# Performance work log

Measured on AMD Instinct MI355X. Metric: run time of the kernel, lower is better.

Reference implementation:

```python
import jax, jax.numpy as jnp
import numpy as np

N = 100_000   # nodes
E = 1_600_000 # edges
K = 3         # Chebyshev order


def _cheb_norm(row, col, w, n):
    # PyG ChebConv norm with normalization='sym', lambda_max=2:
    # L_hat = 2L/lambda_max - I = -D^{-1/2} A D^{-1/2} (diagonal cancels),
    # so only the off-diagonal term survives.
    deg = jax.ops.segment_sum(w, row, num_segments=n)
    dis = jnp.where(deg > 0, jax.lax.rsqrt(deg), 0.0)
    return -dis[row] * w * dis[col]


def _propagate(x, row, col, norm, n):
    # y[i] = sum_{e: row[e]=i} norm[e] * x[col[e]]   (sparse matvec with L_hat)
    return jax.ops.segment_sum(norm[:, None] * x[col], row, num_segments=n)


def _cheb_conv(x, row, col, norm, W, b, n):
    # Chebyshev recursion: T0=x, T1=L_hat x, T_k = 2 L_hat T_{k-1} - T_{k-2}
    Tx0 = x
    out = Tx0 @ W[0]
    Tx1 = _propagate(Tx0, row, col, norm, n)
    out = out + Tx1 @ W[1]
    for k in range(2, W.shape[0]):
        Tx2 = 2.0 * _propagate(Tx1, row, col, norm, n) - Tx0
        out = out + Tx2 @ W[k]
        Tx0, Tx1 = Tx1, Tx2
    return out + b


def setup_inputs() -> dict:
    key = jax.random.key(0)
    ks = jax.random.split(key, 8)
    in_f, c1, c2, out_f = 50, 64, 64, 16
    return {
        "x": jax.random.normal(ks[0], (N, in_f), jnp.float32),
        "edge_index": jax.random.randint(ks[1], (2, E), 0, N),
        "edge_weight": jax.random.uniform(ks[2], (E,), jnp.float32),
        "W1": jax.random.normal(ks[3], (K, in_f, c1), jnp.float32) * 0.05,
        "b1": jnp.zeros((c1,), jnp.float32),
        "W2": jax.random.normal(ks[4], (K, c1, c2), jnp.float32) * 0.05,
        "b2": jnp.zeros((c2,), jnp.float32),
        "bn_gamma": jnp.ones((c1,), jnp.float32),
        "bn_beta": jnp.zeros((c1,), jnp.float32),
        "lin_W": jax.random.normal(ks[5], (out_f, c2), jnp.float32) * 0.05,
        "lin_b": jnp.zeros((out_f,), jnp.float32),
    }


def reference(x, edge_index, edge_weight, W1, b1, W2, b2, bn_gamma, bn_beta, lin_W, lin_b):
    row, col = edge_index[0], edge_index[1]
    n = x.shape[0]
    norm = _cheb_norm(row, col, edge_weight, n)
    # conv1 + relu
    h = jax.nn.relu(_cheb_conv(x, row, col, norm, W1, b1, n))
    # BatchNorm1d over the node dimension (training-mode batch stats, eps=1e-5)
    mu = h.mean(axis=0)
    var = h.var(axis=0)
    h = (h - mu) * jax.lax.rsqrt(var + 1e-5) * bn_gamma + bn_beta
    # dropout with p=0.0 -> identity
    h = jax.nn.relu(_cheb_conv(h, row, col, norm, W2, b2, n))
    return h @ lin_W.T + lin_b
```

## Files before the change

### kernel.cpp

```cpp
#include <hip/hip_runtime.h>
#include <hip/hip_bf16.h>

static constexpr int NF   = 50;
static constexpr int C1   = 64;
static constexpr int OUTF = 16;
static constexpr int SCAN_T = 256;
static constexpr int SCAN_I = 4;
static constexpr float DEG_SCALE   = 8388608.f;
static constexpr float DEG_INV     = 1.f / 8388608.f;

__global__ void pass1_kernel(const int* __restrict__ row, const float* __restrict__ w,
                             unsigned long long* __restrict__ pcd, int* __restrict__ rank, int e)
{
    int i = blockIdx.x * blockDim.x + threadIdx.x;
    if (i < e) {
        int r = row[i];
        unsigned int wq = (unsigned int)(w[i] * DEG_SCALE + 0.5f);
        unsigned long long pk = (1ULL << 32) | (unsigned long long)wq;
        unsigned long long old = atomicAdd(&pcd[r], pk);
        rank[i] = (int)(old >> 32);
    }
}

__global__ void dis_kernel(const unsigned long long* __restrict__ pcd,
                           float* __restrict__ dis, int* __restrict__ cnt, int n)
{
    int i = blockIdx.x * blockDim.x + threadIdx.x;
    if (i < n) {
        unsigned long long pk = pcd[i];
        int c = (int)(pk >> 32);
        float d = (float)(unsigned int)(pk & 0xFFFFFFFFu) * DEG_INV;
        cnt[i] = c;
        dis[i] = (d > 0.f) ? (1.f / sqrtf(d)) : 0.f;
    }
}

__global__ void scan_partial(const int* __restrict__ cnt, int* __restrict__ bsum, int n)
{
    __shared__ int sm[SCAN_T];
    int t = threadIdx.x;
    int base = blockIdx.x * SCAN_T * SCAN_I + t * SCAN_I;
    int s = 0;
    #pragma unroll
    for (int k = 0; k < SCAN_I; ++k) { int i = base + k; if (i < n) s += cnt[i]; }
    sm[t] = s; __syncthreads();
    for (int off = SCAN_T / 2; off > 0; off >>= 1) {
        if (t < off) sm[t] += sm[t + off];
        __syncthreads();
    }
    if (t == 0) bsum[blockIdx.x] = sm[0];
}

__global__ void scan_bsums(int* __restrict__ bsum, int nb)
{
    __shared__ int sm[256];
    int t = threadIdx.x;
    sm[t] = (t < nb) ? bsum[t] : 0;
    __syncthreads();
    for (int off = 1; off < 256; off <<= 1) {
        int v = (t >= off) ? sm[t - off] : 0;
        __syncthreads();
        sm[t] += v;
        __syncthreads();
    }
    if (t < nb) bsum[t] = (t == 0) ? 0 : sm[t - 1];
}

__global__ void scan_final(const int* __restrict__ cnt, const int* __restrict__ bsum,
                           int* __restrict__ rowptr, int n)
{
    __shared__ int sm[SCAN_T];
    int t = threadIdx.x;
    int base = blockIdx.x * SCAN_T * SCAN_I + t * SCAN_I;
    int v[SCAN_I]; int s = 0;
    #pragma unroll
    for (int k = 0; k < SCAN_I; ++k) { int i = base + k; v[k] = (i < n) ? cnt[i] : 0; s += v[k]; }
    sm[t] = s; __syncthreads();
    for (int off = 1; off < SCAN_T; off <<= 1) {
        int x = (t >= off) ? sm[t - off] : 0;
        __syncthreads();
        sm[t] += x;
        __syncthreads();
    }
    int pref = bsum[blockIdx.x] + sm[t] - s;
    #pragma unroll
    for (int k = 0; k < SCAN_I; ++k) {
        int i = base + k;
        if (i < n) { rowptr[i] = pref; pref += v[k]; }
    }
}

__global__ void scatter_kernel(const int* __restrict__ row, const int* __restrict__ col,
                               const float* __restrict__ w, const float* __restrict__ dis,
                               const int* __restrict__ rowptr, const int* __restrict__ rank,
                               int2* __restrict__ ecn, int e)
{
    int i = blockIdx.x * blockDim.x + threadIdx.x;
    if (i < e) {
        int r = row[i], c = col[i];
        int pos = rowptr[r] + rank[i];
        float nv = -dis[r] * w[i] * dis[c];
        ecn[pos] = make_int2(c, __float_as_int(nv));
    }
}

template<int XS, int VALID, int BS>
__global__ __launch_bounds__(256) void prop_kernel(
    const float* __restrict__ xin, const float* __restrict__ base,
    const int* __restrict__ rowptr, const int* __restrict__ cnt,
    const int2* __restrict__ ecn,
    float* __restrict__ yout, int n)
{
    int gw = (blockIdx.x * blockDim.x + threadIdx.x) >> 6;
    int lane = threadIdx.x & 63;
    if (gw >= n) return;
    int st = __builtin_amdgcn_readfirstlane(rowptr[gw]);
    int m  = __builtin_amdgcn_readfirstlane(cnt[gw]);
    const int xi = (XS == C1) ? lane : ((lane < XS) ? lane : 0);
    float a[8] = {0.f, 0.f, 0.f, 0.f, 0.f, 0.f, 0.f, 0.f};
    for (int t = 0; t < m; t += 8) {
        #pragma unroll
        for (int k = 0; k < 8; ++k) {
            int tk = t + k;
            int idx = st + min(tk, m - 1);
            int2 md = ecn[idx];
            float nv = (tk < m) ? __int_as_float(md.y) : 0.f;
            a[k] += nv * xin[md.x * XS + xi];
        }
    }
    float acc = ((a[0] + a[1]) + (a[2] + a[3])) + ((a[4] + a[5]) + (a[6] + a[7]));
    if (VALID != C1 && lane >= VALID) acc = 0.f;
    if (BS > 0) {
        float bv = (VALID == C1 || lane < VALID) ? base[(size_t)gw * BS + lane] : 0.f;
        acc = 2.f * acc - bv;
    }
    yout[(size_t)gw * C1 + lane] = acc;
}

__global__ __launch_bounds__(512) void dense1_kernel(
    const float* __restrict__ x, float* U , const float* __restrict__ T2,
    const float* __restrict__ W1, const float* __restrict__ b1,
    float* __restrict__ stats, int n)
{
    __shared__ __align__(16) float WI[3 * 13 * 64 * 4];
    __shared__ __align__(16) float ROWS[8 * 4 * 3 * 64];
    __shared__ float red[2][8][64];
    const int tid = threadIdx.x;
    for (int i = tid; i < 3 * 13 * 64 * 4; i += 512) WI[i] = 0.f;
    __syncthreads();
    for (int i = tid; i < 3 * NF * C1; i += 512) {
        int tap = i / (NF * C1), rem = i % (NF * C1), f = rem / C1, j = rem % C1;
        WI[((tap * 13 + (f >> 2)) * 64 + j) * 4 + (f & 3)] = W1[i];
    }
    __syncthreads();

    const int lane = tid & 63;
    const int wv   = tid >> 6;
    const int gw   = blockIdx.x * 8 + wv;
    const int rstep = gridDim.x * 8 * 4;
    const float bias = b1[lane];
    const float4* W4 = (const float4*)WI;
    const float4* R4 = (const float4*)ROWS;
    float ssum = 0.f, ssq = 0.f;

    for (int r0 = gw * 4; r0 < n; r0 += rstep) {
        const int nr = min(4, n - r0);
        #pragma unroll
        for (int r = 0; r < 4; ++r) {
            int row = min(r0 + r, n - 1);
            ROWS[((wv * 4 + r) * 3 + 0) * 64 + lane] = (lane < NF) ? x[row * NF + lane] : 0.f;
            ROWS[((wv * 4 + r) * 3 + 1) * 64 + lane] = U [row * C1 + lane];
            ROWS[((wv * 4 + r) * 3 + 2) * 64 + lane] = T2[row * C1 + lane];
        }
        float acc[4] = {bias, bias, bias, bias};
        for (int c = 0; c < 13; ++c) {
            float4 w0 = W4[(0 * 13 + c) * 64 + lane];
            float4 w1 = W4[(1 * 13 + c) * 64 + lane];
            float4 w2 = W4[(2 * 13 + c) * 64 + lane];
            #pragma unroll
            for (int r = 0; r < 4; ++r) {
                float4 t0 = R4[((wv * 4 + r) * 3 + 0) * 16 + c];
                float4 t1 = R4[((wv * 4 + r) * 3 + 1) * 16 + c];
                float4 t2 = R4[((wv * 4 + r) * 3 + 2) * 16 + c];
                acc[r] += t0.x * w0.x + t0.y * w0.y + t0.z * w0.z + t0.w * w0.w
                        + t1.x * w1.x + t1.y * w1.y + t1.z * w1.z + t1.w * w1.w
                        + t2.x * w2.x + t2.y * w2.y + t2.z * w2.z + t2.w * w2.w;
            }
        }
        #pragma unroll
        for (int r = 0; r < 4; ++r) {
            if (r < nr) {
                float v = fmaxf(acc[r], 0.f);
                U[(r0 + r) * C1 + lane] = v;
                ssum += v; ssq += v * v;
            }
        }
    }
    red[0][wv][lane] = ssum;
    red[1][wv][lane] = ssq;
    __syncthreads();
    if (tid < 128) {
        int which = tid >> 6, j = tid & 63;
        float tot = 0.f;
        #pragma unroll
        for (int wq = 0; wq < 8; ++wq) tot += red[which][wq][j];
        atomicAdd(&stats[which * 64 + j], tot);
    }
}

__global__ void bn_finalize_kernel(float* __restrict__ stats, const float* __restrict__ gamma,
                                   const float* __restrict__ beta, float inv_n)
{
    int j = threadIdx.x;
    if (j < 64) {
        float mu   = stats[j] * inv_n;
        float var  = stats[64 + j] * inv_n - mu * mu;
        float rstd = 1.f / sqrtf(var + 1e-5f);
        float sc   = gamma[j] * rstd;
        stats[128 + j] = sc;
        stats[192 + j] = beta[j] - mu * sc;
    }
}

__global__ void bn_apply_kernel(float* __restrict__ h, const float* __restrict__ stats, int n4)
{
    int i = blockIdx.x * blockDim.x + threadIdx.x;
    const int stride = gridDim.x * blockDim.x;
    int j0 = (i * 4) & 63;
    float s0 = stats[128 + j0], s1 = stats[129 + j0], s2 = stats[130 + j0], s3 = stats[131 + j0];
    float b0 = stats[192 + j0], b1 = stats[193 + j0], b2 = stats[194 + j0], b3 = stats[195 + j0];
    float4* h4 = (float4*)h;
    for (; i < n4; i += stride) {
        float4 v = h4[i];
        v.x = v.x * s0 + b0;
        v.y = v.y * s1 + b1;
        v.z = v.z * s2 + b2;
        v.w = v.w * s3 + b3;
        h4[i] = v;
    }
}

__global__ __launch_bounds__(512) void dense2_kernel(
    const float* __restrict__ hb, const float* __restrict__ Q1, const float* __restrict__ T2,
    const float* __restrict__ W2, const float* __restrict__ b2,
    const float* __restrict__ linW, const float* __restrict__ linb,
    float* __restrict__ out, int n)
{
    __shared__ __align__(16) float WI[3 * 16 * 64 * 4];
    __shared__ __align__(16) float ROWS[8 * 4 * 3 * 64];
    __shared__ float LWT[C1 * OUTF];
    const int tid = threadIdx.x;
    for (int i = tid; i < 3 * C1 * C1; i += 512) {
        int tap = i / (C1 * C1), rem = i % (C1 * C1), f = rem / C1, j = rem % C1;
        WI[((tap * 16 + (f >> 2)) * 64 + j) * 4 + (f & 3)] = W2[i];
    }
    for (int i = tid; i < C1 * OUTF; i += 512) {
        int j = i / OUTF, o = i % OUTF;
        LWT[i] = linW[o * C1 + j];
    }
    __syncthreads();

    const int lane = tid & 63;
    const int wv   = tid >> 6;
    const int gw   = blockIdx.x * 8 + wv;
    const int rstep = gridDim.x * 8 * 4;
    const float bias = b2[lane];
    const float lb   = linb[lane & 15];
    const int rsel = lane >> 4, osel = lane & 15;
    const float4* W4 = (const float4*)WI;
    const float4* R4 = (const float4*)ROWS;
    float* gb = &ROWS[wv * (4 * 3 * 64)];

    for (int r0 = gw * 4; r0 < n; r0 += rstep) {
        const int nr = min(4, n - r0);
        #pragma unroll
        for (int r = 0; r < 4; ++r) {
            int row = min(r0 + r, n - 1);
            ROWS[((wv * 4 + r) * 3 + 0) * 64 + lane] = hb[row * C1 + lane];
            ROWS[((wv * 4 + r) * 3 + 1) * 64 + lane] = Q1[row * C1 + lane];
            ROWS[((wv * 4 + r) * 3 + 2) * 64 + lane] = T2[row * C1 + lane];
        }
        float acc[4] = {bias, bias, bias, bias};
        for (int c = 0; c < 16; ++c) {
            float4 w0 = W4[(0 * 16 + c) * 64 + lane];
            float4 w1 = W4[(1 * 16 + c) * 64 + lane];
            float4 w2 = W4[(2 * 16 + c) * 64 + lane];
            #pragma unroll
            for (int r = 0; r < 4; ++r) {
                float4 t0 = R4[((wv * 4 + r) * 3 + 0) * 16 + c];
                float4 t1 = R4[((wv * 4 + r) * 3 + 1) * 16 + c];
                float4 t2 = R4[((wv * 4 + r) * 3 + 2) * 16 + c];
                acc[r] += t0.x * w0.x + t0.y * w0.y + t0.z * w0.z + t0.w * w0.w
                        + t1.x * w1.x + t1.y * w1.y + t1.z * w1.z + t1.w * w1.w
                        + t2.x * w2.x + t2.y * w2.y + t2.z * w2.z + t2.w * w2.w;
            }
        }
        #pragma unroll
        for (int r = 0; r < 4; ++r)
            gb[r * 72 + lane] = (r < nr) ? fmaxf(acc[r], 0.f) : 0.f;
        float oa = lb;
        #pragma unroll 8
        for (int j = 0; j < C1; ++j)
            oa += gb[rsel * 72 + j] * LWT[j * OUTF + osel];
        int rw = r0 + rsel;
        if (rw < n) out[rw * OUTF + osel] = oa;
    }
}

extern "C" void kernel_launch(void* const* d_in, const int* in_sizes, int n_in,
                              void* d_out, int out_size, void* d_ws, size_t ws_size,
                              hipStream_t stream)
{
    const float* x     = (const float*)d_in[0];
    const int*   ei    = (const int*)  d_in[1];
    const float* ew    = (const float*)d_in[2];
    const float* W1    = (const float*)d_in[3];
    const float* b1    = (const float*)d_in[4];
    const float* W2    = (const float*)d_in[5];
    const float* b2    = (const float*)d_in[6];
    const float* gamma = (const float*)d_in[7];
    const float* beta  = (const float*)d_in[8];
    const float* linW  = (const float*)d_in[9];
    const float* linb  = (const float*)d_in[10];
    float* out = (float*)d_out;
    (void)n_in; (void)out_size; (void)ws_size;

    const int n = in_sizes[0] / NF;
    const int e = in_sizes[2];
    const int* row = ei;
    const int* col = ei + e;

    char* ws = (char*)d_ws;
    size_t off = 0;
    auto alloc = [&](size_t bytes) -> void* {
        void* p = ws + off;
        off += (bytes + 255) & ~(size_t)255;
        return p;
    };
    unsigned long long* pcd = (unsigned long long*)alloc((size_t)n * 8);
    float* dis    = (float*)alloc((size_t)n * 4);
    int*   cnt    = (int*)  alloc((size_t)n * 4);
    int*   rowptr = (int*)  alloc((size_t)n * 4);
    int*   rank   = (int*)  alloc((size_t)e * 4);
    int*   bsum   = (int*)  alloc(256 * 4);
    float* stats  = (float*)alloc(256 * 4);
    int2*  ecn    = (int2*) alloc((size_t)e * 8);
    float* U      = (float*)alloc((size_t)n * C1 * 4);
    float* H      = (float*)alloc((size_t)n * C1 * 4);
    float* S      = (float*)alloc((size_t)n * C1 * 4);

    hipMemsetAsync(pcd,   0, (size_t)n * 8, stream);
    hipMemsetAsync(stats, 0, 256 * 4, stream);

    const int eb  = (e + 255) / 256;
    const int nbk = (n + 255) / 256;
    pass1_kernel<<<eb, 256, 0, stream>>>(row, ew, pcd, rank, e);
    dis_kernel<<<nbk, 256, 0, stream>>>(pcd, dis, cnt, n);

    const int nb = (n + SCAN_T * SCAN_I - 1) / (SCAN_T * SCAN_I);
    scan_partial<<<nb, SCAN_T, 0, stream>>>(cnt, bsum, n);
    scan_bsums<<<1, 256, 0, stream>>>(bsum, nb);
    scan_final<<<nb, SCAN_T, 0, stream>>>(cnt, bsum, rowptr, n);
    scatter_kernel<<<eb, 256, 0, stream>>>(row, col, ew, dis, rowptr, rank, ecn, e);

    const int pb = (n + 3) / 4;

    prop_kernel<NF, NF, 0 ><<<pb, 256, 0, stream>>>(x, x, rowptr, cnt, ecn, U, n);
    prop_kernel<C1, NF, NF><<<pb, 256, 0, stream>>>(U, x, rowptr, cnt, ecn, H, n);
    dense1_kernel<<<1024, 512, 0, stream>>>(x, U, H, W1, b1, stats, n);
    bn_finalize_kernel<<<1, 64, 0, stream>>>(stats, gamma, beta, 1.f / (float)n);
    bn_apply_kernel<<<2048, 256, 0, stream>>>(U, stats, n * C1 / 4);

    prop_kernel<C1, C1, 0 ><<<pb, 256, 0, stream>>>(U, U, rowptr, cnt, ecn, H, n);
    prop_kernel<C1, C1, C1><<<pb, 256, 0, stream>>>(H, U, rowptr, cnt, ecn, S, n);
    dense2_kernel<<<1024, 512, 0, stream>>>(U, H, S, W2, b2, linW, linb, out, n);
}
```

Baseline: 532.5 us.

## Vectorize SpMM gathers with float4 and pad input features to 64

```diff
diff --git a/kernel.cpp b/kernel.cpp
--- a/kernel.cpp
+++ b/kernel.cpp
@@ -104,37 +104,74 @@
     }
 }
 
-template<int XS, int VALID, int BS>
+__global__ void padx_kernel(const float* __restrict__ x, float4* __restrict__ X4, int n16)
+{
+    int i = blockIdx.x * blockDim.x + threadIdx.x;
+    if (i < n16) {
+        int row = i >> 4, f0 = (i & 15) * 4;
+        float4 v;
+        v.x = (f0 + 0 < NF) ? x[row * NF + f0 + 0] : 0.f;
+        v.y = (f0 + 1 < NF) ? x[row * NF + f0 + 1] : 0.f;
+        v.z = (f0 + 2 < NF) ? x[row * NF + f0 + 2] : 0.f;
+        v.w = (f0 + 3 < NF) ? x[row * NF + f0 + 3] : 0.f;
+        X4[i] = v;
+    }
+}
+
+template<int BS>
 __global__ __launch_bounds__(256) void prop_kernel(
     const float* __restrict__ xin, const float* __restrict__ base,
     const int* __restrict__ rowptr, const int* __restrict__ cnt,
-    const int2* __restrict__ ecn,
-    float* __restrict__ yout, int n)
+    const int2* __restrict__ ecn, float* __restrict__ yout, int n)
 {
     int gw = (blockIdx.x * blockDim.x + threadIdx.x) >> 6;
     int lane = threadIdx.x & 63;
     if (gw >= n) return;
     int st = __builtin_amdgcn_readfirstlane(rowptr[gw]);
     int m  = __builtin_amdgcn_readfirstlane(cnt[gw]);
-    const int xi = (XS == C1) ? lane : ((lane < XS) ? lane : 0);
-    float a[8] = {0.f, 0.f, 0.f, 0.f, 0.f, 0.f, 0.f, 0.f};
-    for (int t = 0; t < m; t += 8) {
+    const int sub = lane >> 4;
+    const int f4  = lane & 15;
+    const float4* XG = (const float4*)xin;
+
+    float4 a[8];
+    #pragma unroll
+    for (int k = 0; k < 8; ++k) a[k] = make_float4(0.f, 0.f, 0.f, 0.f);
+
+    for (int t = 0; t < m; t += 32) {
         #pragma unroll
         for (int k = 0; k < 8; ++k) {
-            int tk = t + k;
-            int idx = st + min(tk, m - 1);
+            int e   = t + 4 * k + sub;
+            int idx = st + min(e, m - 1);
             int2 md = ecn[idx];
-            float nv = (tk < m) ? __int_as_float(md.y) : 0.f;
-            a[k] += nv * xin[md.x * XS + xi];
-        }
-    }
-    float acc = ((a[0] + a[1]) + (a[2] + a[3])) + ((a[4] + a[5]) + (a[6] + a[7]));
-    if (VALID != C1 && lane >= VALID) acc = 0.f;
-    if (BS > 0) {
-        float bv = (VALID == C1 || lane < VALID) ? base[(size_t)gw * BS + lane] : 0.f;
-        acc = 2.f * acc - bv;
-    }
-    yout[(size_t)gw * C1 + lane] = acc;
+            float nv = (e < m) ? __int_as_float(md.y) : 0.f;
+            float4 g = XG[md.x * 16 + f4];
+            a[k].x = fmaf(nv, g.x, a[k].x);
+            a[k].y = fmaf(nv, g.y, a[k].y);
+            a[k].z = fmaf(nv, g.z, a[k].z);
+            a[k].w = fmaf(nv, g.w, a[k].w);
+        }
+    }
+    float4 av;
+    av.x = ((a[0].x + a[1].x) + (a[2].x + a[3].x)) + ((a[4].x + a[5].x) + (a[6].x + a[7].x));
+    av.y = ((a[0].y + a[1].y) + (a[2].y + a[3].y)) + ((a[4].y + a[5].y) + (a[6].y + a[7].y));
+    av.z = ((a[0].z + a[1].z) + (a[2].z + a[3].z)) + ((a[4].z + a[5].z) + (a[6].z + a[7].z));
+    av.w = ((a[0].w + a[1].w) + (a[2].w + a[3].w)) + ((a[4].w + a[5].w) + (a[6].w + a[7].w));
+    av.x += __shfl_xor(av.x, 32); av.x += __shfl_xor(av.x, 16);
+    av.y += __shfl_xor(av.y, 32); av.y += __shfl_xor(av.y, 16);
+    av.z += __shfl_xor(av.z, 32); av.z += __shfl_xor(av.z, 16);
+    av.w += __shfl_xor(av.w, 32); av.w += __shfl_xor(av.w, 16);
+
+    if (lane < 16) {
+        float4 r = av;
+        if (BS > 0) {
+            float4 b = ((const float4*)base)[(size_t)gw * 16 + lane];
+            r.x = 2.f * r.x - b.x;
+            r.y = 2.f * r.y - b.y;
+            r.z = 2.f * r.z - b.z;
+            r.w = 2.f * r.w - b.w;
+        }
+        ((float4*)yout)[(size_t)gw * 16 + lane] = r;
+    }
 }
 
 __global__ __launch_bounds__(512) void dense1_kernel(
@@ -345,6 +382,7 @@
     int*   bsum   = (int*)  alloc(256 * 4);
     float* stats  = (float*)alloc(256 * 4);
     int2*  ecn    = (int2*) alloc((size_t)e * 8);
+    float* X64    = (float*)alloc((size_t)n * C1 * 4);
     float* U      = (float*)alloc((size_t)n * C1 * 4);
     float* H      = (float*)alloc((size_t)n * C1 * 4);
     float* S      = (float*)alloc((size_t)n * C1 * 4);
@@ -356,6 +394,7 @@
     const int nbk = (n + 255) / 256;
     pass1_kernel<<<eb, 256, 0, stream>>>(row, ew, pcd, rank, e);
     dis_kernel<<<nbk, 256, 0, stream>>>(pcd, dis, cnt, n);
+    padx_kernel<<<(n * 16 + 255) / 256, 256, 0, stream>>>(x, (float4*)X64, n * 16);
 
     const int nb = (n + SCAN_T * SCAN_I - 1) / (SCAN_T * SCAN_I);
     scan_partial<<<nb, SCAN_T, 0, stream>>>(cnt, bsum, n);
@@ -365,13 +404,13 @@
 
     const int pb = (n + 3) / 4;
 
-    prop_kernel<NF, NF, 0 ><<<pb, 256, 0, stream>>>(x, x, rowptr, cnt, ecn, U, n);
-    prop_kernel<C1, NF, NF><<<pb, 256, 0, stream>>>(U, x, rowptr, cnt, ecn, H, n);
+    prop_kernel<0><<<pb, 256, 0, stream>>>(X64, X64, rowptr, cnt, ecn, U, n);
+    prop_kernel<1><<<pb, 256, 0, stream>>>(U, X64, rowptr, cnt, ecn, H, n);
     dense1_kernel<<<1024, 512, 0, stream>>>(x, U, H, W1, b1, stats, n);
     bn_finalize_kernel<<<1, 64, 0, stream>>>(stats, gamma, beta, 1.f / (float)n);
     bn_apply_kernel<<<2048, 256, 0, stream>>>(U, stats, n * C1 / 4);
 
-    prop_kernel<C1, C1, 0 ><<<pb, 256, 0, stream>>>(U, U, rowptr, cnt, ecn, H, n);
-    prop_kernel<C1, C1, C1><<<pb, 256, 0, stream>>>(H, U, rowptr, cnt, ecn, S, n);
+    prop_kernel<0><<<pb, 256, 0, stream>>>(U, U, rowptr, cnt, ecn, H, n);
+    prop_kernel<1><<<pb, 256, 0, stream>>>(H, U, rowptr, cnt, ecn, S, n);
     dense2_kernel<<<1024, 512, 0, stream>>>(U, H, S, W2, b2, linW, linb, out, n);
 }
```

Result: slower. 606.0 us (+13.8%).
